# Kernel optimization log

Measured on AMD Instinct MI355X. Metric: run time of the kernel, lower is better.

Reference implementation:

```python
import jax, jax.numpy as jnp
import numpy as np

B, T, E, H = 2, 4096, 1024, 16
SEGS = (256, 512, 1024, 2048, 4096)
DILS = (1, 2, 4, 8, 16)
NEG = -1e8  # torchscale uses -1e8 for uncovered / masked lse entries


def setup_inputs() -> dict:
    key = jax.random.key(0)
    ks = jax.random.split(key, 5)
    sc = 0.02
    zb = jnp.zeros((E,), jnp.float32)
    return {
        "x": jax.random.normal(ks[0], (B, T, E), jnp.float32),
        "wq": jax.random.normal(ks[1], (E, E), jnp.float32) * sc,
        "bq": zb,
        "wk": jax.random.normal(ks[2], (E, E), jnp.float32) * sc,
        "bk": zb,
        "wv": jax.random.normal(ks[3], (E, E), jnp.float32) * sc,
        "bv": zb,
        "wo": jax.random.normal(ks[4], (E, E), jnp.float32) * sc,
        "bo": zb,
    }


def _scale_attn(q, k, v, w, r):
    # One LongNet scale: segment length w, dilation ratio r.
    # Head group g = head // (H//r) attends to in-segment positions p with p % r == g
    # (torchscale dense_to_sparse diagonal over (r1, r2)).
    Bq, Tq, Hq, d = q.shape
    n, s, hp = Tq // w, w // r, Hq // r  # segments, sparse length, heads per group

    def gather(x):
        # [B,T,H,d] -> segments [B,n,w,H,d]; split w=(s,r1) (p=l*r+r1) and H=(r2,hp);
        # keep diagonal r1 == r2.
        x = x.reshape(Bq, n, s, r, r, hp, d)
        x = jnp.diagonal(x, axis1=3, axis2=4)          # [B,n,s,hp,d,r]
        return jnp.moveaxis(x, -1, 3).reshape(Bq, n, s, Hq, d)

    qs, ks_, vs = gather(q), gather(k), gather(v)
    scores = jnp.einsum('bnqhd,bnkhd->bnhqk', qs, ks_)
    mask = jnp.tril(jnp.ones((s, s), dtype=bool))       # causal within sparse segment
    scores = jnp.where(mask, scores, NEG)
    lse = jax.scipy.special.logsumexp(scores, axis=-1)  # [B,n,h,q]
    out = jnp.einsum('bnhqk,bnkhd->bnqhd', jax.nn.softmax(scores, axis=-1), vs)

    # Scatter back to dense positions (sparse_to_dense): uncovered -> out 0, lse -1e8.
    eye = jnp.eye(r, dtype=out.dtype)
    out_g = out.reshape(Bq, n, s, r, hp, d)                               # heads as (g, hp)
    dense = jnp.einsum('bnsghd,pg->bnspghd', out_g, eye).reshape(Bq, Tq, Hq, d)
    lse_g = jnp.transpose(lse, (0, 1, 3, 2)).reshape(Bq, n, s, r, hp)     # [B,n,s,g,hp]
    lse_d = jnp.where(eye[:, :, None] > 0, lse_g[:, :, :, None, :, :], NEG)
    return dense, lse_d.reshape(Bq, Tq, Hq)


def reference(x, wq, bq, wk, bk, wv, bv, wo, bo):
    d = E // H
    q = (x @ wq + bq).reshape(B, T, H, d) * (d ** -0.5)
    k = (x @ wk + bk).reshape(B, T, H, d)
    v = (x @ wv + bv).reshape(B, T, H, d)
    outs, lses = [], []
    for w_, r_ in zip(SEGS, DILS):
        o, l = _scale_attn(q, k, v, w_, r_)
        outs.append(o)
        lses.append(l)
    # Merge scales with softmax over per-scale log-sum-exp (dense-attention equivalence).
    wgt = jax.nn.softmax(jnp.stack(lses), axis=0)[..., None]  # [S,B,T,H,1]
    y = jnp.sum(jnp.stack(outs) * wgt, axis=0).reshape(B, T, E)
    return y @ wo + bo
```

## Files before the change

kernel.cpp:

```cpp
#include <hip/hip_runtime.h>
#include <hip/hip_bf16.h>

typedef __bf16 bf16_t;
typedef __bf16 bf16x8 __attribute__((ext_vector_type(8)));
typedef __bf16 bf16x4 __attribute__((ext_vector_type(4)));
typedef float f32x4 __attribute__((ext_vector_type(4)));
typedef int vint4 __attribute__((ext_vector_type(4)));

#define AS1 __attribute__((address_space(1)))
#define AS3 __attribute__((address_space(3)))

constexpr int B_ = 2, T_ = 4096, E_ = 1024, H_ = 16;
constexpr int M_ = B_ * T_;

__device__ constexpr size_t OB_OFF[5]  = {0, 8388608, 12582912, 14680064, 15728640};
__device__ constexpr size_t LSE_OFF[5] = {0, 131072, 196608, 229376, 245760};
constexpr size_t OB_TOTAL  = 16252928;
constexpr size_t LSE_TOTAL = 253952;

__global__ __launch_bounds__(256) void cvt_f32_bf16(const float* __restrict__ in,
                                                    bf16_t* __restrict__ out) {
  int i = (blockIdx.x * 256 + threadIdx.x) * 4;
  const float4 v = *(const float4*)(in + i);
  bf16x4 o;
  o[0] = (bf16_t)v.x; o[1] = (bf16_t)v.y; o[2] = (bf16_t)v.z; o[3] = (bf16_t)v.w;
  *(bf16x4*)(out + i) = o;
}

__global__ __launch_bounds__(256) void cvt_transpose_w(
    const float* __restrict__ w0, const float* __restrict__ w1,
    const float* __restrict__ w2, const float* __restrict__ w3,
    bf16_t* __restrict__ o0, bf16_t* __restrict__ o1,
    bf16_t* __restrict__ o2, bf16_t* __restrict__ o3) {
  __shared__ float tile[32][33];
  const float* src; bf16_t* dst;
  switch (blockIdx.z) {
    case 0: src = w0; dst = o0; break;
    case 1: src = w1; dst = o1; break;
    case 2: src = w2; dst = o2; break;
    default: src = w3; dst = o3; break;
  }
  const int n0 = blockIdx.x * 32, k0 = blockIdx.y * 32;
  const int tx = threadIdx.x & 31, ty = threadIdx.x >> 5;
#pragma unroll
  for (int i = 0; i < 32; i += 8)
    tile[ty + i][tx] = src[(size_t)(k0 + ty + i) * E_ + n0 + tx];
  __syncthreads();
#pragma unroll
  for (int i = 0; i < 32; i += 8)
    dst[(size_t)(n0 + ty + i) * E_ + k0 + tx] = (bf16_t)tile[tx][ty + i];
}

template <bool OUT_BF16, bool QKV>
__global__ __launch_bounds__(256, 4) void gemm_bt(
    const bf16_t* __restrict__ A, const bf16_t* __restrict__ BT,
    const float* __restrict__ bias0, const float* __restrict__ bias1,
    const float* __restrict__ bias2, void* __restrict__ Cout, float qscale) {
  constexpr int K = E_;
  __shared__ bf16_t As[128 * 64];
  __shared__ bf16_t Bs[128 * 64];
  const int tid = threadIdx.x;
  const int lane = tid & 63;
  const int wave = tid >> 6;
  const int wm = wave >> 1, wn = wave & 1;
  const int lc = lane & 15, lg = lane >> 4;
  const int bm = blockIdx.x;
  int bn = blockIdx.y;

  const float* bias = bias0;
  float scale = 1.0f;
  void* outp = Cout;
  const bf16_t* Bt = BT;
  if (QKV) {
    const int which = bn >> 3;
    bn &= 7;
    bias = (which == 0) ? bias0 : (which == 1) ? bias1 : bias2;
    scale = (which == 0) ? qscale : 1.0f;
    outp = (void*)((bf16_t*)Cout + (size_t)which * M_ * E_);
    Bt += (size_t)which * E_ * E_;
  }

  f32x4 acc[4][4] = {};

  const int lrow = tid >> 3;
  const int schunk = (tid & 7) ^ (lrow & 7);
  const bf16_t* Ag = A + (size_t)(bm * 128 + lrow) * K + schunk * 8;
  const bf16_t* Bg = Bt + (size_t)(bn * 128 + lrow) * K + schunk * 8;

  const int sl0 = ((0 * 4 + lg) ^ (lc & 7)) * 8;
  const int sl1 = ((1 * 4 + lg) ^ (lc & 7)) * 8;

  for (int k0 = 0; k0 < K; k0 += 64) {
    __syncthreads();
#pragma unroll
    for (int p = 0; p < 4; ++p) {
      __builtin_amdgcn_global_load_lds(
          (const AS1 void*)(Ag + (size_t)(p * 32) * K + k0),
          (AS3 void*)(As + p * 2048 + tid * 8), 16, 0, 0);
      __builtin_amdgcn_global_load_lds(
          (const AS1 void*)(Bg + (size_t)(p * 32) * K + k0),
          (AS3 void*)(Bs + p * 2048 + tid * 8), 16, 0, 0);
    }
    __syncthreads();
#pragma unroll
    for (int kk = 0; kk < 2; ++kk) {
      const int sl = kk ? sl1 : sl0;
      bf16x8 af[4], bfr[4];
#pragma unroll
      for (int i = 0; i < 4; ++i) {
        af[i]  = *(const bf16x8*)&As[(wm * 64 + i * 16 + lc) * 64 + sl];
        bfr[i] = *(const bf16x8*)&Bs[(wn * 64 + i * 16 + lc) * 64 + sl];
      }
#pragma unroll
      for (int i = 0; i < 4; ++i)
#pragma unroll
        for (int j = 0; j < 4; ++j)
          acc[i][j] = __builtin_amdgcn_mfma_f32_16x16x32_bf16(af[i], bfr[j], acc[i][j], 0, 0, 0);
    }
  }

#pragma unroll
  for (int i = 0; i < 4; ++i) {
    const int row = bm * 128 + wm * 64 + i * 16 + lg * 4;
#pragma unroll
    for (int j = 0; j < 4; ++j) {
      const int col = bn * 128 + wn * 64 + j * 16 + lc;
      const float bv = bias[col];
#pragma unroll
      for (int rg = 0; rg < 4; ++rg) {
        const float v = (acc[i][j][rg] + bv) * scale;
        if (OUT_BF16)
          ((bf16_t*)outp)[(size_t)(row + rg) * E_ + col] = (bf16_t)v;
        else
          ((float*)outp)[(size_t)(row + rg) * E_ + col] = v;
      }
    }
  }
}

template <bool S0>
__global__ __launch_bounds__(512, 4) void attn_inst(
    const bf16_t* __restrict__ Q, const bf16_t* __restrict__ K,
    const bf16_t* __restrict__ V, bf16_t* __restrict__ Ob,
    float* __restrict__ Lse, bf16_t* __restrict__ Y) {
  __shared__ alignas(16) bf16_t Ks[256 * 64];
  __shared__ alignas(16) bf16_t Vt[64 * 256];
  __shared__ alignas(16) bf16_t Pw[8][16][40];

  const int bid = blockIdx.x;
  int s, ibase;
  if (S0) { s = 0; ibase = 0; }
  else if (bid < 256) { s = 1; ibase = 0; }
  else if (bid < 384) { s = 2; ibase = 256; }
  else if (bid < 448) { s = 3; ibase = 384; }
  else                { s = 4; ibase = 448; }
  const int inst = bid - ibase;
  const int h = inst & 15;
  const int nseg_log = 4 - s;
  const int seg = (inst >> 4) & ((1 << nseg_log) - 1);
  const int b = inst >> (4 + nseg_log);
  const int g = h >> (4 - s);

  const int t = threadIdx.x;
  const int lane = t & 63;
  const int wv = t >> 6;
  const int lc = lane & 15;
  const int lg = lane >> 4;

  {
    const int krow = t >> 3;
    const int kch = ((t & 7) ^ (krow & 7)) * 8;
#pragma unroll
    for (int p = 0; p < 4; ++p) {
      const int tk = ((seg * 256 + krow + p * 64) << s) + g;
      __builtin_amdgcn_global_load_lds(
          (const AS1 void*)(K + ((size_t)b * T_ + tk) * E_ + h * 64 + kch),
          (AS3 void*)(Ks + p * 4096 + t * 8), 16, 0, 0);
    }
  }
  {
    const int r0 = (t & 63) * 4;
    const int d0 = (t >> 6) * 8;
    bf16x8 va[4];
#pragma unroll
    for (int rr = 0; rr < 4; ++rr) {
      const int tk = ((seg * 256 + r0 + rr) << s) + g;
      va[rr] = *(const bf16x8*)(V + ((size_t)b * T_ + tk) * E_ + h * 64 + d0);
    }
#pragma unroll
    for (int d = 0; d < 8; ++d) {
      bf16x4 w;
      w[0] = va[0][d]; w[1] = va[1][d]; w[2] = va[2][d]; w[3] = va[3][d];
      *(bf16x4*)&Vt[(d0 + d) * 256 + (r0 ^ ((d & 7) << 3))] = w;
    }
  }
  __syncthreads();

  const size_t rowbase = (size_t)(b * H_ + h) * (T_ >> s) + seg * 256;

#pragma unroll
  for (int sel = 0; sel < 2; ++sel) {
    const int tile = sel ? (15 - wv) : wv;
    const int q = tile * 16 + lc;

    const int tq = ((seg * 256 + q) << s) + g;
    const bf16_t* Qg = Q + ((size_t)b * T_ + tq) * E_ + h * 64 + lg * 8;
    bf16x8 qfrag0 = *(const bf16x8*)(Qg);
    bf16x8 qfrag1 = *(const bf16x8*)(Qg + 32);

    float m = -INFINITY, Z = 0.0f;
    f32x4 Oa[4] = {};

    const int nkb = tile / 4 + 1;
    const int diag = tile / 4;
    const int kxor = (lc & 7);
    for (int kb = 0; kb < nkb; ++kb) {
      f32x4 sacc[4] = {};
      __builtin_amdgcn_s_setprio(1);
#pragma unroll
      for (int kt = 0; kt < 4; ++kt) {
        const int krow = kb * 64 + kt * 16 + lc;
        bf16x8 kf0 = *(const bf16x8*)&Ks[krow * 64 + ((0 + lg) ^ kxor) * 8];
        bf16x8 kf1 = *(const bf16x8*)&Ks[krow * 64 + ((4 + lg) ^ kxor) * 8];
        sacc[kt] = __builtin_amdgcn_mfma_f32_16x16x32_bf16(kf0, qfrag0, sacc[kt], 0, 0, 0);
        sacc[kt] = __builtin_amdgcn_mfma_f32_16x16x32_bf16(kf1, qfrag1, sacc[kt], 0, 0, 0);
      }
      __builtin_amdgcn_s_setprio(0);
      if (kb == diag) {
#pragma unroll
        for (int kt = 0; kt < 4; ++kt)
#pragma unroll
          for (int rg = 0; rg < 4; ++rg)
            if (kb * 64 + kt * 16 + lg * 4 + rg > q) sacc[kt][rg] = -1e30f;
      }
      float pm = -1e30f;
#pragma unroll
      for (int kt = 0; kt < 4; ++kt) {
        pm = fmaxf(pm, fmaxf(fmaxf(sacc[kt][0], sacc[kt][1]),
                             fmaxf(sacc[kt][2], sacc[kt][3])));
      }
      pm = fmaxf(pm, __shfl_xor(pm, 16));
      pm = fmaxf(pm, __shfl_xor(pm, 32));
      if (!__all(pm - m <= 11.5f)) {
        const float nm = fmaxf(m, pm);
        const float crr = __builtin_amdgcn_exp2f(m - nm);
        Z *= crr;
#pragma unroll
        for (int dt = 0; dt < 4; ++dt)
#pragma unroll
          for (int rg = 0; rg < 4; ++rg) Oa[dt][rg] *= crr;
        m = nm;
      }
      float psum = 0.0f;
      bf16x4 pv[4];
#pragma unroll
      for (int kt = 0; kt < 4; ++kt)
#pragma unroll
        for (int rg = 0; rg < 4; ++rg) {
          const float p = __builtin_amdgcn_exp2f(sacc[kt][rg] - m);
          psum += p;
          pv[kt][rg] = (bf16_t)p;
        }
      psum += __shfl_xor(psum, 16);
      psum += __shfl_xor(psum, 32);
      Z += psum;
#pragma unroll
      for (int hf = 0; hf < 2; ++hf) {
        *(bf16x4*)&Pw[wv][lc][lg * 4]      = pv[hf * 2 + 0];
        *(bf16x4*)&Pw[wv][lc][16 + lg * 4] = pv[hf * 2 + 1];
        bf16x8 pb = *(const bf16x8*)&Pw[wv][lc][lg * 8];
        __builtin_amdgcn_s_setprio(1);
#pragma unroll
        for (int dt = 0; dt < 4; ++dt) {
          const int vrow = dt * 16 + lc;
          const int vcol = ((kb * 2 + hf) * 32 + lg * 8) ^ ((lc & 7) << 3);
          bf16x8 vf = *(const bf16x8*)&Vt[vrow * 256 + vcol];
          Oa[dt] = __builtin_amdgcn_mfma_f32_16x16x32_bf16(vf, pb, Oa[dt], 0, 0, 0);
        }
        __builtin_amdgcn_s_setprio(0);
      }
    }

    const float lse = m + __builtin_amdgcn_logf(Z);
    const float iZ = 1.0f / Z;
    if (!S0) {
      bf16_t* orow = Ob + OB_OFF[s] + (rowbase + q) * 64 + lg * 4;
#pragma unroll
      for (int dt = 0; dt < 4; ++dt) {
        bf16x4 ov;
        ov[0] = (bf16_t)(Oa[dt][0] * iZ);
        ov[1] = (bf16_t)(Oa[dt][1] * iZ);
        ov[2] = (bf16_t)(Oa[dt][2] * iZ);
        ov[3] = (bf16_t)(Oa[dt][3] * iZ);
        *(bf16x4*)(orow + dt * 16) = ov;
      }
      if (lg == 0) Lse[LSE_OFF[s] + rowbase + q] = lse;
    } else {
      const int t_glob = seg * 256 + q;
      float l2v[4];
      bf16x4 ovv[4][4];
#pragma unroll
      for (int s2 = 1; s2 <= 4; ++s2) {
        const size_t idx = (size_t)(b * H_ + h) * (T_ >> s2) + (t_glob >> s2);
        l2v[s2 - 1] = Lse[LSE_OFF[s2] + idx];
        const bf16_t* orow = Ob + OB_OFF[s2] + idx * 64 + lg * 4;
#pragma unroll
        for (int dt = 0; dt < 4; ++dt)
          ovv[s2 - 1][dt] = *(const bf16x4*)(orow + dt * 16);
      }
      float o16[4][4];
#pragma unroll
      for (int dt = 0; dt < 4; ++dt)
#pragma unroll
        for (int rg = 0; rg < 4; ++rg) o16[dt][rg] = Oa[dt][rg] * iZ;
      float M = lse, S = 1.0f;
#pragma unroll
      for (int s2 = 1; s2 <= 4; ++s2) {
        const int r = 1 << s2;
        const int gg = h >> (4 - s2);
        const bool cov = ((t_glob & (r - 1)) == gg);
        const float l2 = cov ? l2v[s2 - 1] : -INFINITY;
        const float nM = fmaxf(M, l2);
        const float a = __builtin_amdgcn_exp2f(M - nM);
        const float e = __builtin_amdgcn_exp2f(l2 - nM);
#pragma unroll
        for (int dt = 0; dt < 4; ++dt)
#pragma unroll
          for (int rg = 0; rg < 4; ++rg)
            o16[dt][rg] = o16[dt][rg] * a + (float)ovv[s2 - 1][dt][rg] * e;
        S = S * a + e;
        M = nM;
      }
      const float invS = 1.0f / S;
      bf16_t* yrow = Y + ((size_t)b * T_ + t_glob) * E_ + h * 64 + lg * 4;
#pragma unroll
      for (int dt = 0; dt < 4; ++dt) {
        bf16x4 ov;
        ov[0] = (bf16_t)(o16[dt][0] * invS);
        ov[1] = (bf16_t)(o16[dt][1] * invS);
        ov[2] = (bf16_t)(o16[dt][2] * invS);
        ov[3] = (bf16_t)(o16[dt][3] * invS);
        *(bf16x4*)(yrow + dt * 16) = ov;
      }
    }
  }
}

extern "C" void kernel_launch(void* const* d_in, const int* in_sizes, int n_in,
                              void* d_out, int out_size, void* d_ws, size_t ws_size,
                              hipStream_t stream) {
  (void)in_sizes; (void)n_in; (void)out_size; (void)ws_size;
  const float* x  = (const float*)d_in[0];
  const float* wq = (const float*)d_in[1];
  const float* bq = (const float*)d_in[2];
  const float* wk = (const float*)d_in[3];
  const float* bk = (const float*)d_in[4];
  const float* wv = (const float*)d_in[5];
  const float* bv = (const float*)d_in[6];
  const float* wo = (const float*)d_in[7];
  const float* bo = (const float*)d_in[8];

  char* p = (char*)d_ws;
  auto take = [&](size_t bytes) {
    char* q = p;
    p += (bytes + 255) & ~(size_t)255;
    return (void*)q;
  };
  bf16_t* wq_t = (bf16_t*)take((size_t)E_ * E_ * 2);
  bf16_t* wk_t = (bf16_t*)take((size_t)E_ * E_ * 2);
  bf16_t* wv_t = (bf16_t*)take((size_t)E_ * E_ * 2);
  bf16_t* wo_t = (bf16_t*)take((size_t)E_ * E_ * 2);
  bf16_t* xb   = (bf16_t*)take((size_t)M_ * E_ * 2);
  bf16_t* qb   = (bf16_t*)take((size_t)M_ * E_ * 2);
  bf16_t* kbuf = (bf16_t*)take((size_t)M_ * E_ * 2);
  bf16_t* vbuf = (bf16_t*)take((size_t)M_ * E_ * 2);
  bf16_t* yb   = (bf16_t*)take((size_t)M_ * E_ * 2);
  bf16_t* Ob   = (bf16_t*)take(OB_TOTAL * 2);
  float*  Lse  = (float*)take(LSE_TOTAL * 4);
  (void)wk_t; (void)wv_t;

  cvt_f32_bf16<<<M_ * E_ / 1024, 256, 0, stream>>>(x, xb);
  cvt_transpose_w<<<dim3(32, 32, 4), 256, 0, stream>>>(wq, wk, wv, wo, wq_t, wk_t, wv_t, wo_t);

  gemm_bt<true, true><<<dim3(M_ / 128, 24), 256, 0, stream>>>(
      xb, wq_t, bq, bk, bv, qb, 0.125f * 1.44269504f);

  attn_inst<false><<<480, 512, 0, stream>>>(qb, kbuf, vbuf, Ob, Lse, yb);
  attn_inst<true><<<512, 512, 0, stream>>>(qb, kbuf, vbuf, Ob, Lse, yb);

  gemm_bt<false, false><<<dim3(M_ / 128, 8), 256, 0, stream>>>(
      yb, wo_t, bo, bo, bo, d_out, 1.0f);
}
```

Before: 127.9 us.

## Software-pipeline PV MFMA behind next block's QK and defer row-sum reduction

The P·V matrix multiply for each key block is delayed to the next iteration, so it issues right after that iteration's QK MFMAs, with an epilogue for the last block. This is meant to hide softmax exp and LDS write latency behind matrix work. The row-sum cross-lane shuffles now happen once at the end rather than every block. The P scratch buffer is changed to an XOR-swizzled 64-wide layout. Costs are higher register pressure and the buffer reuse relying on in-wave ordering.

```diff
diff --git a/kernel.cpp b/kernel.cpp
--- a/kernel.cpp
+++ b/kernel.cpp
@@ -145,7 +145,7 @@
     float* __restrict__ Lse, bf16_t* __restrict__ Y) {
   __shared__ alignas(16) bf16_t Ks[256 * 64];
   __shared__ alignas(16) bf16_t Vt[64 * 256];
-  __shared__ alignas(16) bf16_t Pw[8][16][40];
+  __shared__ alignas(16) bf16_t Pw[8 * 16 * 64];
 
   const int bid = blockIdx.x;
   int s, ibase;
@@ -197,6 +197,8 @@
   __syncthreads();
 
   const size_t rowbase = (size_t)(b * H_ + h) * (T_ >> s) + seg * 256;
+  bf16_t* PwRow = &Pw[wv * 1024 + lc * 64];
+  const int kxor = (lc & 7);
 
 #pragma unroll
   for (int sel = 0; sel < 2; ++sel) {
@@ -208,12 +210,11 @@
     bf16x8 qfrag0 = *(const bf16x8*)(Qg);
     bf16x8 qfrag1 = *(const bf16x8*)(Qg + 32);
 
-    float m = -INFINITY, Z = 0.0f;
+    float m = -INFINITY, Zp = 0.0f;
     f32x4 Oa[4] = {};
 
     const int nkb = tile / 4 + 1;
     const int diag = tile / 4;
-    const int kxor = (lc & 7);
     for (int kb = 0; kb < nkb; ++kb) {
       f32x4 sacc[4] = {};
       __builtin_amdgcn_s_setprio(1);
@@ -225,6 +226,19 @@
         sacc[kt] = __builtin_amdgcn_mfma_f32_16x16x32_bf16(kf0, qfrag0, sacc[kt], 0, 0, 0);
         sacc[kt] = __builtin_amdgcn_mfma_f32_16x16x32_bf16(kf1, qfrag1, sacc[kt], 0, 0, 0);
       }
+      if (kb > 0) {
+#pragma unroll
+        for (int hf = 0; hf < 2; ++hf) {
+          bf16x8 pb = *(const bf16x8*)&PwRow[(hf * 32 + lg * 8) ^ (kxor * 8)];
+#pragma unroll
+          for (int dt = 0; dt < 4; ++dt) {
+            const int vrow = dt * 16 + lc;
+            const int vcol = (((kb - 1) * 2 + hf) * 32 + lg * 8) ^ (kxor << 3);
+            bf16x8 vf = *(const bf16x8*)&Vt[vrow * 256 + vcol];
+            Oa[dt] = __builtin_amdgcn_mfma_f32_16x16x32_bf16(vf, pb, Oa[dt], 0, 0, 0);
+          }
+        }
+      }
       __builtin_amdgcn_s_setprio(0);
       if (kb == diag) {
 #pragma unroll
@@ -244,43 +258,42 @@
       if (!__all(pm - m <= 11.5f)) {
         const float nm = fmaxf(m, pm);
         const float crr = __builtin_amdgcn_exp2f(m - nm);
-        Z *= crr;
+        Zp *= crr;
 #pragma unroll
         for (int dt = 0; dt < 4; ++dt)
 #pragma unroll
           for (int rg = 0; rg < 4; ++rg) Oa[dt][rg] *= crr;
         m = nm;
       }
-      float psum = 0.0f;
-      bf16x4 pv[4];
-#pragma unroll
-      for (int kt = 0; kt < 4; ++kt)
+#pragma unroll
+      for (int kt = 0; kt < 4; ++kt) {
+        bf16x4 pv;
 #pragma unroll
         for (int rg = 0; rg < 4; ++rg) {
           const float p = __builtin_amdgcn_exp2f(sacc[kt][rg] - m);
-          psum += p;
-          pv[kt][rg] = (bf16_t)p;
+          Zp += p;
+          pv[rg] = (bf16_t)p;
         }
-      psum += __shfl_xor(psum, 16);
-      psum += __shfl_xor(psum, 32);
-      Z += psum;
-#pragma unroll
-      for (int hf = 0; hf < 2; ++hf) {
-        *(bf16x4*)&Pw[wv][lc][lg * 4]      = pv[hf * 2 + 0];
-        *(bf16x4*)&Pw[wv][lc][16 + lg * 4] = pv[hf * 2 + 1];
-        bf16x8 pb = *(const bf16x8*)&Pw[wv][lc][lg * 8];
-        __builtin_amdgcn_s_setprio(1);
-#pragma unroll
-        for (int dt = 0; dt < 4; ++dt) {
-          const int vrow = dt * 16 + lc;
-          const int vcol = ((kb * 2 + hf) * 32 + lg * 8) ^ ((lc & 7) << 3);
-          bf16x8 vf = *(const bf16x8*)&Vt[vrow * 256 + vcol];
-          Oa[dt] = __builtin_amdgcn_mfma_f32_16x16x32_bf16(vf, pb, Oa[dt], 0, 0, 0);
-        }
-        __builtin_amdgcn_s_setprio(0);
-      }
-    }
-
+        const int clog = (kt >> 1) * 32 + (kt & 1) * 16 + lg * 4;
+        *(bf16x4*)&PwRow[clog ^ (kxor << 3)] = pv;
+      }
+    }
+    __builtin_amdgcn_s_setprio(1);
+#pragma unroll
+    for (int hf = 0; hf < 2; ++hf) {
+      bf16x8 pb = *(const bf16x8*)&PwRow[(hf * 32 + lg * 8) ^ (kxor * 8)];
+#pragma unroll
+      for (int dt = 0; dt < 4; ++dt) {
+        const int vrow = dt * 16 + lc;
+        const int vcol = (((nkb - 1) * 2 + hf) * 32 + lg * 8) ^ (kxor << 3);
+        bf16x8 vf = *(const bf16x8*)&Vt[vrow * 256 + vcol];
+        Oa[dt] = __builtin_amdgcn_mfma_f32_16x16x32_bf16(vf, pb, Oa[dt], 0, 0, 0);
+      }
+    }
+    __builtin_amdgcn_s_setprio(0);
+
+    float Z = Zp + __shfl_xor(Zp, 16);
+    Z = Z + __shfl_xor(Z, 32);
     const float lse = m + __builtin_amdgcn_logf(Z);
     const float iZ = 1.0f / Z;
     if (!S0) {
```

Measured after the change: 127.5 us. Within noise of the previous version (-0.3%).
